# Performance work log

Hardware: AMD Instinct MI355X
Metric: run time of the kernel (lower is better)

Reference implementation:

```python
import jax, jax.numpy as jnp
import numpy as np

B, N, C, NH, R = 8, 4096, 256, 8, 4
HH = WW = 64
D = C // NH
EPS_LN = 1e-5
EPS_ATT = 1e-6


def layernorm(x, g, b):
    m = jnp.mean(x, axis=-1, keepdims=True)
    v = jnp.var(x, axis=-1, keepdims=True)
    return (x - m) * jax.lax.rsqrt(v + EPS_LN) * g + b


def setup_inputs() -> dict:
    key = jax.random.key(0)
    ks = jax.random.split(key, 12)
    s = 0.02
    return {
        "x": jax.random.normal(ks[0], (B, N, C), jnp.float32),
        "sr_w": jax.random.normal(ks[1], (C, C, R, R), jnp.float32) * s,  # OIHW
        "sr_b": jnp.zeros((C,), jnp.float32),
        "norm_g": jnp.ones((C,), jnp.float32),
        "norm_b": jnp.zeros((C,), jnp.float32),
        "wq": jax.random.normal(ks[2], (C, C), jnp.float32) * s,
        "wk": jax.random.normal(ks[3], (C, C), jnp.float32) * s,
        "wv": jax.random.normal(ks[4], (C, C), jnp.float32) * s,
        "wm": jax.random.normal(ks[5], (C, C), jnp.float32) * s,
        "mlp_w1": jax.random.normal(ks[6], (2 * C, 2 * C), jnp.float32) * s,
        "mlp_w2": jax.random.normal(ks[7], (C, 2 * C), jnp.float32) * s,
        "norm1_g": jnp.ones((C,), jnp.float32),
        "norm1_b": jnp.zeros((C,), jnp.float32),
        "norm2_g": jnp.ones((C,), jnp.float32),
        "norm2_b": jnp.zeros((C,), jnp.float32),
        "H": HH,
        "W": WW,
    }


def reference(x, sr_w, sr_b, norm_g, norm_b, wq, wk, wv, wm, mlp_w1, mlp_w2,
              norm1_g, norm1_b, norm2_g, norm2_b, H, W):
    Bs, Np, Cc = x.shape
    query_in = x
    # --- strided-conv subsample (kernel=stride=R, VALID) + LayerNorm ---
    xi = jnp.transpose(x, (0, 2, 1)).reshape(Bs, Cc, H, W)
    xs = jax.lax.conv_general_dilated(xi, sr_w, window_strides=(R, R), padding='VALID',
                                      dimension_numbers=('NCHW', 'OIHW', 'NCHW'))
    xs = xs + sr_b[None, :, None, None]
    src = jnp.transpose(xs.reshape(Bs, Cc, -1), (0, 2, 1))  # [B, S, C]
    src = layernorm(src, norm_g, norm_b)
    # --- LoFTR encoder layer: QKV proj + linear (elu+1) attention ---
    q = (query_in @ wq.T).reshape(Bs, -1, NH, D)
    k = (src @ wk.T).reshape(Bs, -1, NH, D)
    v = (src @ wv.T).reshape(Bs, -1, NH, D)
    Q = jax.nn.elu(q) + 1.0
    K = jax.nn.elu(k) + 1.0
    S = v.shape[1]
    v_scaled = v / S
    KV = jnp.einsum('bshd,bshv->bhdv', K, v_scaled)          # [B,H,D,D]
    Z = 1.0 / (jnp.einsum('blhd,bhd->blh', Q, K.sum(axis=1)) + EPS_ATT)
    msg = jnp.einsum('blhd,bhdv,blh->blhv', Q, KV, Z) * S    # [B,L,H,D]
    # --- merge + norm1 + concat MLP + norm2 + residual ---
    msg = msg.reshape(Bs, -1, Cc) @ wm.T
    msg = layernorm(msg, norm1_g, norm1_b)
    h = jnp.concatenate([query_in, msg], axis=2) @ mlp_w1.T
    h = jax.nn.relu(h) @ mlp_w2.T
    h = layernorm(h, norm2_g, norm2_b)
    return query_in + h
```

## Files before the change

### kernel.cpp

```cpp
#include <hip/hip_runtime.h>
#include <hip/hip_bf16.h>
#include <math.h>

#define B_   8
#define N_   4096
#define C_   256
#define NH_  8
#define D_   32
#define S_   256
#define HH_  64

#define BM 128
#define BN 128
#define BK 32
#define NSLICE 16

typedef __bf16 bf16x8 __attribute__((ext_vector_type(8)));
typedef float f32x4 __attribute__((ext_vector_type(4)));

__device__ inline ushort f2b(float f) {
    __hip_bfloat16 h = __float2bfloat16(f);
    return *reinterpret_cast<ushort*>(&h);
}
__device__ inline float b2f(ushort u) {
    unsigned v = (unsigned)u << 16;
    union { unsigned u; float f; } c; c.u = v; return c.f;
}

__device__ inline void gload16(const void* g, void* l) {
    __builtin_amdgcn_global_load_lds(
        (const __attribute__((address_space(1))) unsigned int*)g,
        (__attribute__((address_space(3))) unsigned int*)l, 16, 0, 0);
}

#define NSEG 7
struct CastArgs {
    const float* s[NSEG];
    ushort*      d[NSEG];
    int          n4[NSEG];
    int          total4;
};
__global__ __launch_bounds__(256) void cast_w_kernel(CastArgs a) {
    int idx = blockIdx.x * 256 + threadIdx.x;
    if (idx >= a.total4) return;
    int i = idx, s = 0;
    while (i >= a.n4[s]) { i -= a.n4[s]; ++s; }
    float4 f = ((const float4*)a.s[s])[i];
    ushort4 o;
    o.x = f2b(f.x); o.y = f2b(f.y); o.z = f2b(f.z); o.w = f2b(f.w);
    ((ushort4*)a.d[s])[i] = o;
}

__global__ __launch_bounds__(256) void gather_kernel(const float* __restrict__ x,
                                                     ushort* __restrict__ P,
                                                     ushort* __restrict__ cat) {
    int bs = blockIdx.x;
    int b = bs >> 8, s = bs & 255;
    int i = s >> 4, j = s & 15;
    int c = threadIdx.x;
    const float* xb = x + (size_t)b * N_ * C_;
    ushort u[16];
#pragma unroll
    for (int pq = 0; pq < 16; ++pq) {
        int p = pq >> 2, q = pq & 3;
        int n = (i * 4 + p) * HH_ + (j * 4 + q);
        float f = xb[(size_t)n * C_ + c];
        u[pq] = f2b(f);
        cat[((size_t)(b * N_ + n)) * 512 + c] = u[pq];
    }
    ushort* dst = P + (size_t)bs * 4096 + c * 16;
    ((uint4*)dst)[0] = *(uint4*)&u[0];
    ((uint4*)dst)[1] = *(uint4*)&u[8];
}

__global__ __launch_bounds__(512) void gemm_bf16(
    const ushort* __restrict__ A, int lda,
    const ushort* __restrict__ W, int ldw,
    float* __restrict__ Cf, ushort* __restrict__ Cb, int ldc,
    int Kchunk, int act, long spstride)
{
    __shared__ ushort As[2 * BM * BK];
    __shared__ ushort Bs[2 * BN * BK];
    const int t = threadIdx.x;
    const int lane = t & 63;
    const int w = t >> 6;
    const int wr = w >> 2, wc = w & 3;
    const int fr = lane & 15, fq = lane >> 4;
    const int bm = blockIdx.x * BM, bn = blockIdx.y * BN;
    const long koff = (long)blockIdx.z * Kchunk;

    f32x4 acc[4][2] = {};

    const ushort* Ag = A + (size_t)bm * lda + koff;
    const ushort* Wg = W + (size_t)bn * ldw + koff;
    char* AsB = (char*)As;
    char* BsB = (char*)Bs;
    const int wuni = (t & ~63) * 16;

    const int srow = t >> 2;
    const int skb0 = ((t & 3) * 8) ^ ((srow & 3) * 8);

    auto STAGE = [&](int buf, int k0) {
        gload16(Ag + (size_t)srow * lda + k0 + skb0, AsB + buf * 8192 + wuni);
        gload16(Wg + (size_t)srow * ldw + k0 + skb0, BsB + buf * 8192 + wuni);
    };

    STAGE(0, 0);
    __syncthreads();
    int cur = 0;
    for (int k0 = 0; k0 < Kchunk; k0 += BK) {
        if (k0 + BK < Kchunk) STAGE(cur ^ 1, k0 + BK);

        const ushort* Ac = As + cur * (BM * BK);
        const ushort* Bc = Bs + cur * (BN * BK);
        bf16x8 af[4], bv[2];
#pragma unroll
        for (int m = 0; m < 4; ++m) {
            int ra = wr * 64 + m * 16 + fr;
            af[m] = *(const bf16x8*)&Ac[ra * BK + (fq * 8 ^ ((ra & 3) * 8))];
        }
#pragma unroll
        for (int n = 0; n < 2; ++n) {
            int rb = wc * 32 + n * 16 + fr;
            bv[n] = *(const bf16x8*)&Bc[rb * BK + (fq * 8 ^ ((rb & 3) * 8))];
        }
#pragma unroll
        for (int m = 0; m < 4; ++m)
#pragma unroll
            for (int n = 0; n < 2; ++n)
                acc[m][n] = __builtin_amdgcn_mfma_f32_16x16x32_bf16(
                    af[m], bv[n], acc[m][n], 0, 0, 0);

        __syncthreads();
        cur ^= 1;
    }

    float* Cfz = Cf ? Cf + (size_t)blockIdx.z * spstride : nullptr;
#pragma unroll
    for (int m = 0; m < 4; ++m) {
#pragma unroll
        for (int n = 0; n < 2; ++n) {
            int col = bn + wc * 32 + n * 16 + fr;
#pragma unroll
            for (int i = 0; i < 4; ++i) {
                int row = bm + wr * 64 + m * 16 + fq * 4 + i;
                float v = acc[m][n][i];
                if (act == 1 || (act == 3 && col < 256))
                    v = v > 0.f ? v + 1.f : __expf(v);
                else if (act == 2) v = fmaxf(v, 0.f);
                if (Cb) Cb[(size_t)row * ldc + col] = f2b(v);
                else    Cfz[(size_t)row * ldc + col] = v;
            }
        }
    }
}

__global__ __launch_bounds__(256) void ln_reduce_kernel(
    const float* __restrict__ part,
    const float* __restrict__ bias,
    const float* __restrict__ g, const float* __restrict__ bvec,
    ushort* __restrict__ outb)
{
    int row = blockIdx.x * 4 + (threadIdx.x >> 6);
    int lane = threadIdx.x & 63;
    int c0 = lane * 4;
    float4 v = *(const float4*)&bias[c0];
#pragma unroll
    for (int s = 0; s < NSLICE; ++s) {
        float4 p = *(const float4*)&part[(size_t)s * 2048 * 256 + (size_t)row * 256 + c0];
        v.x += p.x; v.y += p.y; v.z += p.z; v.w += p.w;
    }
    float s1 = v.x + v.y + v.z + v.w;
    float s2 = v.x * v.x + v.y * v.y + v.z * v.z + v.w * v.w;
#pragma unroll
    for (int m = 1; m < 64; m <<= 1) {
        s1 += __shfl_xor(s1, m);
        s2 += __shfl_xor(s2, m);
    }
    float mean = s1 * (1.f / C_);
    float rstd = rsqrtf(s2 * (1.f / C_) - mean * mean + 1e-5f);
    float4 gv = *(const float4*)&g[c0];
    float4 bb = *(const float4*)&bvec[c0];
    ushort4 o;
    o.x = f2b((v.x - mean) * rstd * gv.x + bb.x);
    o.y = f2b((v.y - mean) * rstd * gv.y + bb.y);
    o.z = f2b((v.z - mean) * rstd * gv.z + bb.z);
    o.w = f2b((v.w - mean) * rstd * gv.w + bb.w);
    *(ushort4*)&outb[(size_t)row * C_ + c0] = o;
}

__global__ __launch_bounds__(256) void ln_kernel(
    const ushort* __restrict__ inb,
    const float* __restrict__ g, const float* __restrict__ bvec,
    const float* __restrict__ residual,
    float* __restrict__ outf, ushort* __restrict__ outb, int ldout)
{
    int row = blockIdx.x * 4 + (threadIdx.x >> 6);
    int lane = threadIdx.x & 63;
    int c0 = lane * 4;
    ushort4 u = *(const ushort4*)&inb[(size_t)row * C_ + c0];
    float x0 = b2f(u.x), x1 = b2f(u.y), x2 = b2f(u.z), x3 = b2f(u.w);
    float s1 = x0 + x1 + x2 + x3;
    float s2 = x0 * x0 + x1 * x1 + x2 * x2 + x3 * x3;
#pragma unroll
    for (int m = 1; m < 64; m <<= 1) {
        s1 += __shfl_xor(s1, m);
        s2 += __shfl_xor(s2, m);
    }
    float mean = s1 * (1.f / C_);
    float rstd = rsqrtf(s2 * (1.f / C_) - mean * mean + 1e-5f);
    float4 gv = *(const float4*)&g[c0];
    float4 bb = *(const float4*)&bvec[c0];
    float y0 = (x0 - mean) * rstd * gv.x + bb.x;
    float y1 = (x1 - mean) * rstd * gv.y + bb.y;
    float y2 = (x2 - mean) * rstd * gv.z + bb.z;
    float y3 = (x3 - mean) * rstd * gv.w + bb.w;
    if (residual) {
        float4 r = *(const float4*)&residual[(size_t)row * C_ + c0];
        y0 += r.x; y1 += r.y; y2 += r.z; y3 += r.w;
    }
    if (outb) {
        ushort4 o; o.x = f2b(y0); o.y = f2b(y1); o.z = f2b(y2); o.w = f2b(y3);
        *(ushort4*)&outb[(size_t)row * ldout + c0] = o;
    } else {
        *(float4*)&outf[(size_t)row * ldout + c0] = make_float4(y0, y1, y2, y3);
    }
}

__global__ __launch_bounds__(256) void kv_kernel(const ushort* __restrict__ kvin,
                                                 float* __restrict__ KV,
                                                 float* __restrict__ Ksum) {
    int bh = blockIdx.x;
    int b = bh >> 3, h = bh & 7;
    const ushort* Kp = kvin + (size_t)b * S_ * 512 + h * D_;
    const ushort* Vp = Kp + 256;
    int tid = threadIdx.x;
    __shared__ float Ks[8][32], Vs[8][32];
    int d = tid >> 3, vq = tid & 7;
    int ls = tid >> 5, lc = tid & 31;
    float acc[4] = {0.f, 0.f, 0.f, 0.f};
    float ks = 0.f;
    for (int s0 = 0; s0 < S_; s0 += 8) {
        __syncthreads();
        Ks[ls][lc] = b2f(Kp[(size_t)(s0 + ls) * 512 + lc]);
        Vs[ls][lc] = b2f(Vp[(size_t)(s0 + ls) * 512 + lc]);
        __syncthreads();
#pragma unroll
        for (int ss = 0; ss < 8; ++ss) {
            float kd = Ks[ss][d];
            if (vq == 0) ks += kd;
#pragma unroll
            for (int jj = 0; jj < 4; ++jj)
                acc[jj] += kd * Vs[ss][vq * 4 + jj];
        }
    }
    float* kvout = KV + ((size_t)bh * 32 + d) * 32 + vq * 4;
#pragma unroll
    for (int jj = 0; jj < 4; ++jj) kvout[jj] = acc[jj];
    if (vq == 0) Ksum[bh * 32 + d] = ks;
}

__global__ __launch_bounds__(256) void msg_kernel(const ushort* __restrict__ Q,
                                                  const float* __restrict__ KV,
                                                  const float* __restrict__ Ksum,
                                                  ushort* __restrict__ out) {
    const int row0 = blockIdx.x * 64;
    const int b = row0 >> 12;
    const int tid = threadIdx.x;
    const int h = tid >> 5, v = tid & 31;
    __shared__ float KVs[8192];
    __shared__ float Kss[256];
    __shared__ ushort Qs[8][256];
    const float4* kvsrc = (const float4*)(KV + (size_t)b * 8192);
#pragma unroll
    for (int i = 0; i < 8; ++i)
        ((float4*)KVs)[i * 256 + tid] = kvsrc[i * 256 + tid];
    if (tid < 64)
        ((float4*)Kss)[tid] = ((const float4*)(Ksum + b * 256))[tid];
    __syncthreads();
    float kvr[32], ksr[32];
#pragma unroll
    for (int d = 0; d < 32; ++d) {
        kvr[d] = KVs[h * 1024 + d * 32 + v];
        ksr[d] = Kss[h * 32 + d];
    }
    for (int r0 = 0; r0 < 64; r0 += 8) {
        __syncthreads();
        { int r = tid >> 5, c8 = (tid & 31) * 8;
          *(uint4*)&Qs[r][c8] = *(const uint4*)&Q[(size_t)(row0 + r0 + r) * 256 + c8]; }
        __syncthreads();
#pragma unroll
        for (int r = 0; r < 8; ++r) {
            ushort q[32];
            *(uint4*)&q[0]  = *(const uint4*)&Qs[r][h * 32 + 0];
            *(uint4*)&q[8]  = *(const uint4*)&Qs[r][h * 32 + 8];
            *(uint4*)&q[16] = *(const uint4*)&Qs[r][h * 32 + 16];
            *(uint4*)&q[24] = *(const uint4*)&Qs[r][h * 32 + 24];
            float z = 1e-6f, m = 0.f;
#pragma unroll
            for (int d = 0; d < 32; ++d) {
                float qd = b2f(q[d]);
                z = fmaf(qd, ksr[d], z);
                m = fmaf(qd, kvr[d], m);
            }
            out[(size_t)(row0 + r0 + r) * 256 + tid] = f2b(m / z);
        }
    }
}

extern "C" void kernel_launch(void* const* d_in, const int* in_sizes, int n_in,
                              void* d_out, int out_size, void* d_ws, size_t ws_size,
                              hipStream_t stream) {
    const float* x      = (const float*)d_in[0];
    const float* sr_w   = (const float*)d_in[1];
    const float* sr_b   = (const float*)d_in[2];
    const float* norm_g = (const float*)d_in[3];
    const float* norm_b = (const float*)d_in[4];
    const float* wq     = (const float*)d_in[5];
    const float* wk     = (const float*)d_in[6];
    const float* wv     = (const float*)d_in[7];
    const float* wm     = (const float*)d_in[8];
    const float* w1     = (const float*)d_in[9];
    const float* w2     = (const float*)d_in[10];
    const float* n1g    = (const float*)d_in[11];
    const float* n1b    = (const float*)d_in[12];
    const float* n2g    = (const float*)d_in[13];
    const float* n2b    = (const float*)d_in[14];
    float* out = (float*)d_out;

    char* base = (char*)d_ws;
    size_t off = 0;
    auto alloc = [&](size_t bytes) {
        char* p = base + off;
        off += (bytes + 1023) & ~(size_t)1023;
        return p;
    };
    ushort* P16      = (ushort*)alloc(2048ull * 4096 * 2);
    float*  partial  = (float*) alloc((size_t)NSLICE * 2048 * 256 * 4);
    ushort* cat      = (ushort*)alloc(32768ull * 512 * 2);
    ushort* src16    = (ushort*)alloc(2048ull * 256 * 2);
    ushort* kv16     = (ushort*)alloc(2048ull * 512 * 2);
    ushort* qbuf16   = (ushort*)alloc(32768ull * 256 * 2);
    ushort* msg16    = (ushort*)alloc(32768ull * 256 * 2);
    ushort* merged16 = (ushort*)alloc(32768ull * 256 * 2);
    ushort* h1_16    = (ushort*)alloc(32768ull * 512 * 2);
    float*  KV       = (float*) alloc(64ull * 32 * 32 * 4);
    float*  Ksum     = (float*) alloc(64ull * 32 * 4);
    ushort* srw16    = (ushort*)alloc(1048576ull * 2);
    ushort* wq16     = (ushort*)alloc(65536ull * 2);
    ushort* wkv16    = (ushort*)alloc(131072ull * 2);
    ushort* wm16     = (ushort*)alloc(65536ull * 2);
    ushort* w1_16    = (ushort*)alloc(262144ull * 2);
    ushort* w2_16    = (ushort*)alloc(131072ull * 2);
    ushort* h2_16 = P16;

    CastArgs ca;
    ca.s[0] = sr_w; ca.d[0] = srw16;         ca.n4[0] = 1048576 / 4;
    ca.s[1] = wq;   ca.d[1] = wq16;          ca.n4[1] = 65536 / 4;
    ca.s[2] = wk;   ca.d[2] = wkv16;         ca.n4[2] = 65536 / 4;
    ca.s[3] = wv;   ca.d[3] = wkv16 + 65536; ca.n4[3] = 65536 / 4;
    ca.s[4] = wm;   ca.d[4] = wm16;          ca.n4[4] = 65536 / 4;
    ca.s[5] = w1;   ca.d[5] = w1_16;         ca.n4[5] = 262144 / 4;
    ca.s[6] = w2;   ca.d[6] = w2_16;         ca.n4[6] = 131072 / 4;
    ca.total4 = (1048576 + 4 * 65536 + 262144 + 131072) / 4;
    cast_w_kernel<<<(ca.total4 + 255) / 256, 256, 0, stream>>>(ca);

    gather_kernel<<<2048, 256, 0, stream>>>(x, P16, cat);

    { dim3 g(2048 / BM, 256 / BN, NSLICE);
      gemm_bf16<<<g, 512, 0, stream>>>(P16, 4096, srw16, 4096,
                                       partial, nullptr, 256, 4096 / NSLICE, 0, 2048l * 256); }
    ln_reduce_kernel<<<512, 256, 0, stream>>>(partial, sr_b, norm_g, norm_b, src16);

    { dim3 g(2048 / BM, 512 / BN);
      gemm_bf16<<<g, 512, 0, stream>>>(src16, 256, wkv16, 256, nullptr, kv16, 512, 256, 3, 0); }
    { dim3 g(32768 / BM, 256 / BN);
      gemm_bf16<<<g, 512, 0, stream>>>(cat, 512, wq16, 256, nullptr, qbuf16, 256, 256, 1, 0); }

    kv_kernel<<<64, 256, 0, stream>>>(kv16, KV, Ksum);
    msg_kernel<<<512, 256, 0, stream>>>(qbuf16, KV, Ksum, msg16);

    { dim3 g(32768 / BM, 256 / BN);
      gemm_bf16<<<g, 512, 0, stream>>>(msg16, 256, wm16, 256, nullptr, merged16, 256, 256, 0, 0); }
    ln_kernel<<<8192, 256, 0, stream>>>(merged16, n1g, n1b, nullptr,
                                        nullptr, cat + 256, 512);

    { dim3 g(32768 / BM, 512 / BN);
      gemm_bf16<<<g, 512, 0, stream>>>(cat, 512, w1_16, 512, nullptr, h1_16, 512, 512, 2, 0); }
    { dim3 g(32768 / BM, 256 / BN);
      gemm_bf16<<<g, 512, 0, stream>>>(h1_16, 512, w2_16, 512, nullptr, h2_16, 256, 512, 0, 0); }

    ln_kernel<<<8192, 256, 0, stream>>>(h2_16, n2g, n2b, x, out, nullptr, 256);
}
```

Measured before the change: 279.3 us.

## Add full-row GEMM kernel fusing LayerNorm and residual epilogues

Adds a 64x256 tile GEMM that covers the whole 256-column output row per block. This lets the merge projection fuse LayerNorm1 and the second MLP projection fuse LayerNorm2 plus the residual add directly in the epilogue, using a cross-wave shared-memory row reduction. The separate LN kernels and their bf16 intermediate round-trips through global memory are removed. The Q projection also moves to the new kernel, and buffers are aliased to reuse workspace. The trade-off is a smaller M tile with a wider N tile, which changes occupancy and reuse. LayerNorm now also runs on fp32 accumulators instead of bf16-rounded values.

Result: no change. 277.0 us (-0.8%).

```diff
diff --git a/kernel.cpp b/kernel.cpp
--- a/kernel.cpp
+++ b/kernel.cpp
@@ -155,6 +155,137 @@
     }
 }
 
+__global__ __launch_bounds__(512) void gemm_wide(
+    const ushort* __restrict__ A, int lda,
+    const ushort* __restrict__ W, int ldw,
+    int K, int act, int mode,
+    ushort* __restrict__ outb, int ldo,
+    float* __restrict__ outf,
+    const float* __restrict__ g, const float* __restrict__ bvec,
+    const float* __restrict__ resid)
+{
+    __shared__ ushort As[2 * 64 * 32];
+    __shared__ ushort Bs[2 * 256 * 32];
+    __shared__ float2 rs[4][64];
+    const int t = threadIdx.x;
+    const int lane = t & 63;
+    const int w = t >> 6;
+    const int wr = w >> 2, wc = w & 3;
+    const int fr = lane & 15, fq = lane >> 4;
+    const int bm = blockIdx.x * 64;
+
+    f32x4 acc[2][4] = {};
+    const ushort* Ag = A + (size_t)bm * lda;
+    char* AsB = (char*)As;
+    char* BsB = (char*)Bs;
+    const int wuni = (t & ~63) * 16;
+
+    const int srow = t >> 2;
+    const int skb = ((t & 3) * 8) ^ ((srow & 3) * 8);
+
+    auto STAGE = [&](int buf, int k0) {
+        gload16(W + (size_t)srow * ldw + k0 + skb, BsB + buf * 16384 + wuni);
+        gload16(W + (size_t)(128 + srow) * ldw + k0 + skb,
+                BsB + buf * 16384 + 8192 + wuni);
+        if (t < 256)
+            gload16(Ag + (size_t)srow * lda + k0 + skb, AsB + buf * 4096 + wuni);
+    };
+
+    STAGE(0, 0);
+    __syncthreads();
+    int cur = 0;
+    for (int k0 = 0; k0 < K; k0 += BK) {
+        if (k0 + BK < K) STAGE(cur ^ 1, k0 + BK);
+
+        const ushort* Ac = As + cur * (64 * 32);
+        const ushort* Bc = Bs + cur * (256 * 32);
+        bf16x8 af[2], bv[4];
+#pragma unroll
+        for (int m = 0; m < 2; ++m) {
+            int ra = wr * 32 + m * 16 + fr;
+            af[m] = *(const bf16x8*)&Ac[ra * 32 + (fq * 8 ^ ((ra & 3) * 8))];
+        }
+#pragma unroll
+        for (int n = 0; n < 4; ++n) {
+            int rb = wc * 64 + n * 16 + fr;
+            bv[n] = *(const bf16x8*)&Bc[rb * 32 + (fq * 8 ^ ((rb & 3) * 8))];
+        }
+#pragma unroll
+        for (int m = 0; m < 2; ++m)
+#pragma unroll
+            for (int n = 0; n < 4; ++n)
+                acc[m][n] = __builtin_amdgcn_mfma_f32_16x16x32_bf16(
+                    af[m], bv[n], acc[m][n], 0, 0, 0);
+
+        __syncthreads();
+        cur ^= 1;
+    }
+
+    if (mode == 0) {
+#pragma unroll
+        for (int m = 0; m < 2; ++m)
+#pragma unroll
+            for (int n = 0; n < 4; ++n) {
+                int col = wc * 64 + n * 16 + fr;
+#pragma unroll
+                for (int i = 0; i < 4; ++i) {
+                    int row = bm + wr * 32 + m * 16 + fq * 4 + i;
+                    float v = acc[m][n][i];
+                    if (act == 1) v = v > 0.f ? v + 1.f : __expf(v);
+                    else if (act == 2) v = fmaxf(v, 0.f);
+                    outb[(size_t)row * ldo + col] = f2b(v);
+                }
+            }
+        return;
+    }
+
+#pragma unroll
+    for (int m = 0; m < 2; ++m)
+#pragma unroll
+        for (int i = 0; i < 4; ++i) {
+            float s = 0.f, q = 0.f;
+#pragma unroll
+            for (int n = 0; n < 4; ++n) {
+                float v = acc[m][n][i];
+                s += v; q += v * v;
+            }
+#pragma unroll
+            for (int msk = 1; msk < 16; msk <<= 1) {
+                s += __shfl_xor(s, msk);
+                q += __shfl_xor(q, msk);
+            }
+            if (fr == 0)
+                rs[wc][wr * 32 + m * 16 + fq * 4 + i] = make_float2(s, q);
+        }
+    __syncthreads();
+#pragma unroll
+    for (int m = 0; m < 2; ++m)
+#pragma unroll
+        for (int i = 0; i < 4; ++i) {
+            int r64 = wr * 32 + m * 16 + fq * 4 + i;
+            float S = 0.f, Q = 0.f;
+#pragma unroll
+            for (int c4 = 0; c4 < 4; ++c4) {
+                float2 p = rs[c4][r64];
+                S += p.x; Q += p.y;
+            }
+            float mean = S * (1.f / C_);
+            float rstd = rsqrtf(Q * (1.f / C_) - mean * mean + 1e-5f);
+            int row = bm + r64;
+#pragma unroll
+            for (int n = 0; n < 4; ++n) {
+                int col = wc * 64 + n * 16 + fr;
+                float y = (acc[m][n][i] - mean) * rstd * g[col] + bvec[col];
+                if (mode == 1) {
+                    outb[(size_t)row * ldo + col] = f2b(y);
+                } else {
+                    y += resid[(size_t)row * 256 + col];
+                    outf[(size_t)row * 256 + col] = y;
+                }
+            }
+        }
+}
+
 __global__ __launch_bounds__(256) void ln_reduce_kernel(
     const float* __restrict__ part,
     const float* __restrict__ bias,
@@ -187,44 +318,6 @@
     o.z = f2b((v.z - mean) * rstd * gv.z + bb.z);
     o.w = f2b((v.w - mean) * rstd * gv.w + bb.w);
     *(ushort4*)&outb[(size_t)row * C_ + c0] = o;
-}
-
-__global__ __launch_bounds__(256) void ln_kernel(
-    const ushort* __restrict__ inb,
-    const float* __restrict__ g, const float* __restrict__ bvec,
-    const float* __restrict__ residual,
-    float* __restrict__ outf, ushort* __restrict__ outb, int ldout)
-{
-    int row = blockIdx.x * 4 + (threadIdx.x >> 6);
-    int lane = threadIdx.x & 63;
-    int c0 = lane * 4;
-    ushort4 u = *(const ushort4*)&inb[(size_t)row * C_ + c0];
-    float x0 = b2f(u.x), x1 = b2f(u.y), x2 = b2f(u.z), x3 = b2f(u.w);
-    float s1 = x0 + x1 + x2 + x3;
-    float s2 = x0 * x0 + x1 * x1 + x2 * x2 + x3 * x3;
-#pragma unroll
-    for (int m = 1; m < 64; m <<= 1) {
-        s1 += __shfl_xor(s1, m);
-        s2 += __shfl_xor(s2, m);
-    }
-    float mean = s1 * (1.f / C_);
-    float rstd = rsqrtf(s2 * (1.f / C_) - mean * mean + 1e-5f);
-    float4 gv = *(const float4*)&g[c0];
-    float4 bb = *(const float4*)&bvec[c0];
-    float y0 = (x0 - mean) * rstd * gv.x + bb.x;
-    float y1 = (x1 - mean) * rstd * gv.y + bb.y;
-    float y2 = (x2 - mean) * rstd * gv.z + bb.z;
-    float y3 = (x3 - mean) * rstd * gv.w + bb.w;
-    if (residual) {
-        float4 r = *(const float4*)&residual[(size_t)row * C_ + c0];
-        y0 += r.x; y1 += r.y; y2 += r.z; y3 += r.w;
-    }
-    if (outb) {
-        ushort4 o; o.x = f2b(y0); o.y = f2b(y1); o.z = f2b(y2); o.w = f2b(y3);
-        *(ushort4*)&outb[(size_t)row * ldout + c0] = o;
-    } else {
-        *(float4*)&outf[(size_t)row * ldout + c0] = make_float4(y0, y1, y2, y3);
-    }
 }
 
 __global__ __launch_bounds__(256) void kv_kernel(const ushort* __restrict__ kvin,
@@ -340,9 +433,6 @@
     ushort* cat      = (ushort*)alloc(32768ull * 512 * 2);
     ushort* src16    = (ushort*)alloc(2048ull * 256 * 2);
     ushort* kv16     = (ushort*)alloc(2048ull * 512 * 2);
-    ushort* qbuf16   = (ushort*)alloc(32768ull * 256 * 2);
-    ushort* msg16    = (ushort*)alloc(32768ull * 256 * 2);
-    ushort* merged16 = (ushort*)alloc(32768ull * 256 * 2);
     ushort* h1_16    = (ushort*)alloc(32768ull * 512 * 2);
     float*  KV       = (float*) alloc(64ull * 32 * 32 * 4);
     float*  Ksum     = (float*) alloc(64ull * 32 * 4);
@@ -352,7 +442,8 @@
     ushort* wm16     = (ushort*)alloc(65536ull * 2);
     ushort* w1_16    = (ushort*)alloc(262144ull * 2);
     ushort* w2_16    = (ushort*)alloc(131072ull * 2);
-    ushort* h2_16 = P16;
+    ushort* qbuf16 = (ushort*)partial;
+    ushort* msg16  = P16;
 
     CastArgs ca;
     ca.s[0] = sr_w; ca.d[0] = srw16;         ca.n4[0] = 1048576 / 4;
@@ -374,21 +465,17 @@
 
     { dim3 g(2048 / BM, 512 / BN);
       gemm_bf16<<<g, 512, 0, stream>>>(src16, 256, wkv16, 256, nullptr, kv16, 512, 256, 3, 0); }
-    { dim3 g(32768 / BM, 256 / BN);
-      gemm_bf16<<<g, 512, 0, stream>>>(cat, 512, wq16, 256, nullptr, qbuf16, 256, 256, 1, 0); }
+    gemm_wide<<<512, 512, 0, stream>>>(cat, 512, wq16, 256, 256, 1, 0,
+                                       qbuf16, 256, nullptr, nullptr, nullptr, nullptr);
 
     kv_kernel<<<64, 256, 0, stream>>>(kv16, KV, Ksum);
     msg_kernel<<<512, 256, 0, stream>>>(qbuf16, KV, Ksum, msg16);
 
-    { dim3 g(32768 / BM, 256 / BN);
-      gemm_bf16<<<g, 512, 0, stream>>>(msg16, 256, wm16, 256, nullptr, merged16, 256, 256, 0, 0); }
-    ln_kernel<<<8192, 256, 0, stream>>>(merged16, n1g, n1b, nullptr,
-                                        nullptr, cat + 256, 512);
+    gemm_wide<<<512, 512, 0, stream>>>(msg16, 256, wm16, 256, 256, 0, 1,
+                                       cat + 256, 512, nullptr, n1g, n1b, nullptr);
 
     { dim3 g(32768 / BM, 512 / BN);
       gemm_bf16<<<g, 512, 0, stream>>>(cat, 512, w1_16, 512, nullptr, h1_16, 512, 512, 2, 0); }
-    { dim3 g(32768 / BM, 256 / BN);
-      gemm_bf16<<<g, 512, 0, stream>>>(h1_16, 512, w2_16, 512, nullptr, h2_16, 256, 512, 0, 0); }
-
-    ln_kernel<<<8192, 256, 0, stream>>>(h2_16, n2g, n2b, x, out, nullptr, 256);
-}
+    gemm_wide<<<512, 512, 0, stream>>>(h1_16, 512, w2_16, 512, 512, 0, 2,
+                                       nullptr, 0, out, n2g, n2b, x);
+}
```
